# Kernel tuning notes

Measured on AMD Instinct MI355X. Metric: run time of the kernel, lower is better.

The kernel has to match this reference:

```python
import jax, jax.numpy as jnp
import numpy as np

NUM_HEADS = 32
NUM_KV_HEADS = 8
HEAD_DIM = 128
ROPE_THETA = 1000000.0
SCALING = HEAD_DIM ** -0.5


def apply_rope_neox(x, positions):
    # x: [T, H, D], positions: [T] int
    half = HEAD_DIM // 2
    inv_freq = 1.0 / (ROPE_THETA ** (jnp.arange(0, half, dtype=jnp.float32) / half))
    freqs = positions.astype(jnp.float32)[:, None] * inv_freq[None, :]  # [T, D/2]
    cos = jnp.cos(freqs)[:, None, :]  # [T, 1, D/2]
    sin = jnp.sin(freqs)[:, None, :]
    x1, x2 = x[..., :half], x[..., half:]
    return jnp.concatenate([x1 * cos - x2 * sin, x2 * cos + x1 * sin], axis=-1)


def setup_inputs() -> dict:
    key = jax.random.key(0)
    k1, k2, k3 = jax.random.split(key, 3)
    T, H = 2048, 4096
    positions = jnp.arange(T, dtype=jnp.int32)
    hidden_states = jax.random.normal(k1, (T, H), dtype=jnp.float32)
    Wqkv = jax.random.normal(k2, (H, 6144), dtype=jnp.float32) * 0.02
    Wo = jax.random.normal(k3, (H, H), dtype=jnp.float32) * 0.02
    return {"positions": positions, "hidden_states": hidden_states, "Wqkv": Wqkv, "Wo": Wo}


def reference(positions, hidden_states, Wqkv, Wo):
    T = hidden_states.shape[0]
    q_size = NUM_HEADS * HEAD_DIM
    kv_size = NUM_KV_HEADS * HEAD_DIM
    qkv = hidden_states @ Wqkv  # [T, 6144]
    q = qkv[:, :q_size].reshape(T, NUM_HEADS, HEAD_DIM)
    k = qkv[:, q_size:q_size + kv_size].reshape(T, NUM_KV_HEADS, HEAD_DIM)
    v = qkv[:, q_size + kv_size:].reshape(T, NUM_KV_HEADS, HEAD_DIM)
    q = apply_rope_neox(q, positions)
    k = apply_rope_neox(k, positions)
    # GQA: repeat kv heads to match query heads
    rep = NUM_HEADS // NUM_KV_HEADS
    k = jnp.repeat(k, rep, axis=1)  # [T, H, D]
    v = jnp.repeat(v, rep, axis=1)
    scores = jnp.einsum('thd,shd->hts', q, k) * SCALING  # [H, T, T]
    causal = jnp.tril(jnp.ones((T, T), dtype=bool))
    scores = jnp.where(causal[None], scores, jnp.finfo(scores.dtype).min)
    attn = jax.nn.softmax(scores, axis=-1)
    out = jnp.einsum('hts,shd->thd', attn, v).reshape(T, NUM_HEADS * HEAD_DIM)
    return out @ Wo
```

## Files before the change

### kernel.cpp

```cpp
#include <hip/hip_runtime.h>
#include <math.h>

#define T_TOK 2048
#define HDIM  4096
#define QKVN  6144
#define NHEADS 32
#define HD    128
#define KV_OFF 4096
#define V_OFF  5120
#define SCALE 0.08838834764831843f

typedef __attribute__((ext_vector_type(8))) short short8;
typedef __attribute__((ext_vector_type(4))) float f32x4;
typedef __attribute__((ext_vector_type(16))) float f32x16;

__device__ __forceinline__ ushort f2bf(float f) {
    union { float f; unsigned u; } v; v.f = f;
    unsigned r = v.u + 0x7FFFu + ((v.u >> 16) & 1u);
    return (ushort)(r >> 16);
}

template <int N_, int K_>
__global__ __launch_bounds__(512, 2) void gemm_bf16_8ph(const ushort* __restrict__ A,
                                                        const ushort* __restrict__ B,
                                                        float* __restrict__ C) {
    __shared__ __attribute__((aligned(16))) ushort As[2][2][8192];
    __shared__ __attribute__((aligned(16))) ushort Bs[2][2][8192];

    constexpr int NT = K_ / 64;
    constexpr int NBN = N_ / 256;

    const int nwg = (int)gridDim.x;
    const int bid = (int)blockIdx.x;
    const int swz = (nwg & 7) ? bid : ((bid & 7) * (nwg >> 3) + (bid >> 3));
    const int bm = (swz / NBN) * 256;
    const int bn = (swz % NBN) * 256;

    const int tid = (int)threadIdx.x;
    const int w = tid >> 6;
    const int l = tid & 63;
    const int hfa = w >> 2;
    const int hfb = (w & 3) >> 1;
    const int wbr64 = (w & 1) * 4096;

    const int arc = (l & 15) * 64;
    const int ac0 = ((((l >> 4) << 4)) ^ ((l & 7) << 4)) >> 1;
    const int ac1 = (((1 << 6) | ((l >> 4) << 4)) ^ ((l & 7) << 4)) >> 1;

    const int grow = w * 8 + (l >> 3);
    const int gcol = ((l & 7) ^ (l >> 3)) * 8;
    const ushort* Ag = A + (size_t)(bm + grow) * K_ + gcol;
    const ushort* Bg = B + (size_t)(bn + grow) * K_ + gcol;

    auto ldsA = (__attribute__((address_space(3))) char*)&As[0][0][0];
    auto ldsB = (__attribute__((address_space(3))) char*)&Bs[0][0][0];
    const int wsl = w * 1024;

#define STG2(ldsbase, gsrc, bufi, hfi, kt)                                                              \
    do {                                                                                                \
        __builtin_amdgcn_global_load_lds(                                                               \
            (const __attribute__((address_space(1))) void*)((gsrc) + (size_t)((hfi) * 128) * K_ + (kt) * 64),       \
            (__attribute__((address_space(3))) void*)((ldsbase) + (bufi) * 32768 + (hfi) * 16384 + wsl), 16, 0, 0);  \
        __builtin_amdgcn_global_load_lds(                                                               \
            (const __attribute__((address_space(1))) void*)((gsrc) + (size_t)((hfi) * 128 + 64) * K_ + (kt) * 64),  \
            (__attribute__((address_space(3))) void*)((ldsbase) + (bufi) * 32768 + (hfi) * 16384 + 8192 + wsl), 16, 0, 0); \
    } while (0)

    STG2(ldsB, Bg, 0, 0, 0);
    STG2(ldsB, Bg, 0, 1, 0);
    STG2(ldsA, Ag, 0, 0, 0);
    STG2(ldsA, Ag, 0, 1, 0);
    STG2(ldsB, Bg, 1, 0, 1);
    STG2(ldsB, Bg, 1, 1, 1);
    STG2(ldsA, Ag, 1, 0, 1);
    asm volatile("s_waitcnt vmcnt(6)" ::: "memory");
    __builtin_amdgcn_s_barrier();

    f32x4 acc[8][4];
#pragma unroll
    for (int i = 0; i < 8; i++)
#pragma unroll
        for (int j = 0; j < 4; j++) acc[i][j] = (f32x4){0.f, 0.f, 0.f, 0.f};

    short8 a0[4][2], a1[4][2], bq[4][2];

    int buf = 0;
    for (int t = 0; t < NT; ++t) {
        const int nb = buf ^ 1;
        const ushort* Abuf = &As[buf][hfa][0];
        const ushort* Bbuf = &Bs[buf][hfb][0] + wbr64;

#pragma unroll
        for (int fi = 0; fi < 4; fi++) {
            a0[fi][0] = *(const short8*)(Abuf + fi * 1024 + arc + ac0);
            a0[fi][1] = *(const short8*)(Abuf + fi * 1024 + arc + ac1);
        }
#pragma unroll
        for (int fj = 0; fj < 4; fj++) {
            bq[fj][0] = *(const short8*)(Bbuf + fj * 1024 + arc + ac0);
            bq[fj][1] = *(const short8*)(Bbuf + fj * 1024 + arc + ac1);
        }
        if (t + 1 < NT) STG2(ldsA, Ag, nb, 1, t + 1);
        __builtin_amdgcn_s_barrier();
        __builtin_amdgcn_s_setprio(1);
#pragma unroll
        for (int fi = 0; fi < 4; fi++)
#pragma unroll
            for (int fj = 0; fj < 2; fj++)
#pragma unroll
                for (int s = 0; s < 2; s++)
                    acc[fi][fj] = __builtin_amdgcn_mfma_f32_16x16x32_bf16(a0[fi][s], bq[fj][s], acc[fi][fj], 0, 0, 0);
        __builtin_amdgcn_s_setprio(0);
        __builtin_amdgcn_s_barrier();

        if (t + 2 < NT) STG2(ldsB, Bg, buf, 0, t + 2);
        __builtin_amdgcn_s_barrier();
        __builtin_amdgcn_s_setprio(1);
#pragma unroll
        for (int fi = 0; fi < 4; fi++)
#pragma unroll
            for (int fj = 2; fj < 4; fj++)
#pragma unroll
                for (int s = 0; s < 2; s++)
                    acc[fi][fj] = __builtin_amdgcn_mfma_f32_16x16x32_bf16(a0[fi][s], bq[fj][s], acc[fi][fj], 0, 0, 0);
        __builtin_amdgcn_s_setprio(0);
        __builtin_amdgcn_s_barrier();

#pragma unroll
        for (int fi = 0; fi < 4; fi++) {
            a1[fi][0] = *(const short8*)(Abuf + (fi + 4) * 1024 + arc + ac0);
            a1[fi][1] = *(const short8*)(Abuf + (fi + 4) * 1024 + arc + ac1);
        }
        if (t + 2 < NT) STG2(ldsB, Bg, buf, 1, t + 2);
        __builtin_amdgcn_s_barrier();
        __builtin_amdgcn_s_setprio(1);
#pragma unroll
        for (int fi = 0; fi < 4; fi++)
#pragma unroll
            for (int fj = 2; fj < 4; fj++)
#pragma unroll
                for (int s = 0; s < 2; s++)
                    acc[fi + 4][fj] = __builtin_amdgcn_mfma_f32_16x16x32_bf16(a1[fi][s], bq[fj][s], acc[fi + 4][fj], 0, 0, 0);
        __builtin_amdgcn_s_setprio(0);
        __builtin_amdgcn_s_barrier();

        if (t + 2 < NT) {
            STG2(ldsA, Ag, buf, 0, t + 2);
            asm volatile("s_waitcnt vmcnt(6)" ::: "memory");
        } else {
            asm volatile("s_waitcnt vmcnt(0)" ::: "memory");
        }
        __builtin_amdgcn_s_barrier();
        __builtin_amdgcn_s_setprio(1);
#pragma unroll
        for (int fi = 0; fi < 4; fi++)
#pragma unroll
            for (int fj = 0; fj < 2; fj++)
#pragma unroll
                for (int s = 0; s < 2; s++)
                    acc[fi + 4][fj] = __builtin_amdgcn_mfma_f32_16x16x32_bf16(a1[fi][s], bq[fj][s], acc[fi + 4][fj], 0, 0, 0);
        __builtin_amdgcn_s_setprio(0);
        __builtin_amdgcn_s_barrier();

        buf = nb;
    }
#undef STG2

    const int cn = bn + (w & 3) * 64 + (l & 15);
    const int rm = bm + hfa * 128 + ((l >> 4) << 2);
#pragma unroll
    for (int fi = 0; fi < 8; fi++)
#pragma unroll
        for (int fj = 0; fj < 4; fj++)
#pragma unroll
            for (int r = 0; r < 4; r++)
                C[(size_t)(rm + 16 * fi + r) * N_ + cn + 16 * fj] = acc[fi][fj][r];
}

__global__ __launch_bounds__(256) void cast_bf16(const float* __restrict__ in,
                                                 ushort* __restrict__ outp) {
    const int i = (blockIdx.x * 256 + threadIdx.x) * 4;
    float4 v = *(const float4*)(in + i);
    ushort4 o = {f2bf(v.x), f2bf(v.y), f2bf(v.z), f2bf(v.w)};
    *(ushort4*)(outp + i) = o;
}

template <int K_, int N_>
__global__ __launch_bounds__(256) void transpose_cast(const float* __restrict__ W,
                                                      ushort* __restrict__ WT) {
    __shared__ float T[32 * 65];
    const int k0 = blockIdx.y * 32;
    const int n0 = blockIdx.x * 64;
    const int x = threadIdx.x & 63;
    const int y = threadIdx.x >> 6;
#pragma unroll
    for (int p = 0; p < 8; p++) {
        const int kk = p * 4 + y;
        T[kk * 65 + x] = W[(size_t)(k0 + kk) * N_ + n0 + x];
    }
    __syncthreads();
#pragma unroll
    for (int q = 0; q < 4; q++) {
        const int nl = q * 16 + (threadIdx.x >> 4);
        const int k2 = (threadIdx.x & 15) * 2;
        ushort2 o = {f2bf(T[k2 * 65 + nl]), f2bf(T[(k2 + 1) * 65 + nl])};
        *(ushort2*)&WT[(size_t)(n0 + nl) * K_ + k0 + k2] = o;
    }
}

__global__ __launch_bounds__(256) void rope_cast(const int* __restrict__ pos,
                                                 const float* __restrict__ qkv,
                                                 ushort* __restrict__ qkB) {
    const int t = blockIdx.x;
    const int slot = blockIdx.y * 4 + (threadIdx.x >> 6);
    const int d = threadIdx.x & 63;
    const float p = (float)pos[t];
    const float invf = exp2f(-(float)d * (19.931568569324174f / 64.0f));
    const float f = p * invf;
    const float c = cosf(f), s = sinf(f);
    const float sc = (slot < 32) ? SCALE : 1.0f;
    const float* base = qkv + (size_t)t * QKVN + slot * HD;
    ushort* ob = qkB + (size_t)t * QKVN + slot * HD;
    const float x1 = base[d];
    const float x2 = base[d + 64];
    ob[d]      = f2bf((x1 * c - x2 * s) * sc);
    ob[d + 64] = f2bf((x2 * c + x1 * s) * sc);
}

__global__ __launch_bounds__(256) void vt_cast(const float* __restrict__ qkv,
                                               ushort* __restrict__ Vt) {
    __shared__ float tile[32][33];
    const int t0 = blockIdx.x * 32;
    const int c0 = blockIdx.y * 32;
    const int tx = threadIdx.x & 31;
    const int ty = threadIdx.x >> 5;
#pragma unroll
    for (int i = 0; i < 4; i++) {
        const int tt = ty + 8 * i;
        tile[tt][tx] = qkv[(size_t)(t0 + tt) * QKVN + V_OFF + c0 + tx];
    }
    __syncthreads();
#pragma unroll
    for (int i = 0; i < 4; i++) {
        const int dd = ty + 8 * i;
        Vt[(size_t)(c0 + dd) * 2048 + t0 + tx] = f2bf(tile[tx][dd]);
    }
}

__global__ __launch_bounds__(256, 2) void flash_attn_mfma(
        const ushort* __restrict__ qkB,
        const ushort* __restrict__ Vt,
        ushort* __restrict__ attnB) {
    __shared__ ushort Kf[8 * 512];
    __shared__ ushort Vf[8 * 512];

    const int b = blockIdx.x;
    const int half = b >> 8;
    const int rest = b & 255;
    const int h = rest >> 3;
    const int q8 = rest & 7;
    const int qi = half ? (15 - q8) : q8;
    const int kvh = h >> 2;

    const int tid = threadIdx.x;
    const int w = tid >> 6;
    const int l = tid & 63;
    const int l31 = l & 31;
    const int hf = l >> 5;

    const int qg = qi * 128 + w * 32 + l31;

    short8 qf[8];
    {
        const ushort* qrow = qkB + (size_t)qg * QKVN + h * HD + hf * 8;
#pragma unroll
        for (int kt = 0; kt < 8; kt++)
            qf[kt] = *(const short8*)(qrow + kt * 16);
    }

    f32x16 O[4];
#pragma unroll
    for (int dt = 0; dt < 4; dt++)
#pragma unroll
        for (int r = 0; r < 16; r++) O[dt][r] = 0.f;
    float mcur = -INFINITY, lcur = 0.f;

    const ushort* kbase = qkB + (size_t)l31 * QKVN + KV_OFF + kvh * HD + (2 * w) * 16 + hf * 8;
    const ushort* vbase = Vt + ((size_t)(kvh * 128 + w * 32 + l31)) * 2048 + hf * 8;

    auto ldsK = (__attribute__((address_space(3))) char*)Kf;
    auto ldsV = (__attribute__((address_space(3))) char*)Vf;

    const int nst = 4 * qi + 4;
    const int mylast = 4 * qi + w;

    for (int st = 0; st < nst; st++) {
        __syncthreads();
        {
            const ushort* kg = kbase + (size_t)st * 32 * QKVN;
            __builtin_amdgcn_global_load_lds(
                (const __attribute__((address_space(1))) void*)kg,
                (__attribute__((address_space(3))) void*)(ldsK + (2 * w) * 1024), 16, 0, 0);
            __builtin_amdgcn_global_load_lds(
                (const __attribute__((address_space(1))) void*)(kg + 16),
                (__attribute__((address_space(3))) void*)(ldsK + (2 * w + 1) * 1024), 16, 0, 0);
            const ushort* vg = vbase + st * 32;
            __builtin_amdgcn_global_load_lds(
                (const __attribute__((address_space(1))) void*)vg,
                (__attribute__((address_space(3))) void*)(ldsV + (2 * w) * 1024), 16, 0, 0);
            __builtin_amdgcn_global_load_lds(
                (const __attribute__((address_space(1))) void*)(vg + 16),
                (__attribute__((address_space(3))) void*)(ldsV + (2 * w + 1) * 1024), 16, 0, 0);
        }
        __syncthreads();

        if (st <= mylast) {
            f32x16 S;
#pragma unroll
            for (int r = 0; r < 16; r++) S[r] = 0.f;
#pragma unroll
            for (int kt = 0; kt < 8; kt++) {
                short8 afK = *(const short8*)&Kf[kt * 512 + l * 8];
                S = __builtin_amdgcn_mfma_f32_32x32x16_bf16(afK, qf[kt], S, 0, 0, 0);
            }

            float p[16];
#pragma unroll
            for (int r = 0; r < 16; r++) p[r] = S[r];
            if (st == mylast) {
                const int sb = st * 32 + 4 * hf;
#pragma unroll
                for (int r = 0; r < 16; r++) {
                    const int sg = sb + (r & 3) + 8 * (r >> 2);
                    if (sg > qg) p[r] = -INFINITY;
                }
            }
            float rmax = p[0];
#pragma unroll
            for (int r = 1; r < 16; r++) rmax = fmaxf(rmax, p[r]);
            rmax = fmaxf(rmax, __shfl_xor(rmax, 32));
            const float mnew = fmaxf(mcur, rmax);
            const float alpha = __expf(mcur - mnew);
            float rsum = 0.f;
#pragma unroll
            for (int r = 0; r < 16; r++) {
                p[r] = __expf(p[r] - mnew);
                rsum += p[r];
            }
            rsum += __shfl_xor(rsum, 32);
            lcur = lcur * alpha + rsum;
            mcur = mnew;

#pragma unroll
            for (int dt = 0; dt < 4; dt++)
#pragma unroll
                for (int r = 0; r < 16; r++) O[dt][r] *= alpha;

            unsigned pk[8], rk[8];
#pragma unroll
            for (int g = 0; g < 4; g++) {
                pk[2 * g]     = (unsigned)f2bf(p[4 * g])     | ((unsigned)f2bf(p[4 * g + 1]) << 16);
                pk[2 * g + 1] = (unsigned)f2bf(p[4 * g + 2]) | ((unsigned)f2bf(p[4 * g + 3]) << 16);
            }
#pragma unroll
            for (int i = 0; i < 8; i++) rk[i] = (unsigned)__shfl_xor((int)pk[i], 32);

            short8 Pf[2];
#pragma unroll
            for (int kt2 = 0; kt2 < 2; kt2++) {
                const int g = 2 * kt2 + hf;
                union { unsigned u[4]; short8 s; } cvt;
                cvt.u[0] = hf ? rk[2 * g]     : pk[2 * g];
                cvt.u[1] = hf ? rk[2 * g + 1] : pk[2 * g + 1];
                cvt.u[2] = hf ? pk[2 * g]     : rk[2 * g];
                cvt.u[3] = hf ? pk[2 * g + 1] : rk[2 * g + 1];
                Pf[kt2] = cvt.s;
            }

#pragma unroll
            for (int dt = 0; dt < 4; dt++)
#pragma unroll
                for (int kt2 = 0; kt2 < 2; kt2++) {
                    short8 afV = *(const short8*)&Vf[(dt * 2 + kt2) * 512 + l * 8];
                    O[dt] = __builtin_amdgcn_mfma_f32_32x32x16_bf16(afV, Pf[kt2], O[dt], 0, 0, 0);
                }
        }
    }

    const float inv = 1.0f / lcur;
    ushort* orow = attnB + (size_t)qg * HDIM + h * HD + 4 * hf;
#pragma unroll
    for (int dt = 0; dt < 4; dt++)
#pragma unroll
        for (int rg = 0; rg < 4; rg++) {
            ushort4 o;
            o.x = f2bf(O[dt][4 * rg + 0] * inv);
            o.y = f2bf(O[dt][4 * rg + 1] * inv);
            o.z = f2bf(O[dt][4 * rg + 2] * inv);
            o.w = f2bf(O[dt][4 * rg + 3] * inv);
            *(ushort4*)(orow + dt * 32 + 8 * rg) = o;
        }
}

__global__ __launch_bounds__(256) void rope_kernel(const int* __restrict__ pos,
                                                   float* __restrict__ qkv) {
    const int t = blockIdx.x;
    const int head = blockIdx.y * 4 + (threadIdx.x >> 6);
    const int d = threadIdx.x & 63;
    const float p = (float)pos[t];
    const float invf = exp2f(-(float)d * (19.931568569324174f / 64.0f));
    const float f = p * invf;
    const float c = cosf(f), s = sinf(f);
    float* base = qkv + (size_t)t * QKVN + head * HD;
    const float x1 = base[d];
    const float x2 = base[d + 64];
    base[d]      = x1 * c - x2 * s;
    base[d + 64] = x2 * c + x1 * s;
}

#define DOT4(acc, a, b) acc += (a).x*(b).x + (a).y*(b).y + (a).z*(b).z + (a).w*(b).w
#define FMA4(o, p, v) { (o).x += (p)*(v).x; (o).y += (p)*(v).y; (o).z += (p)*(v).z; (o).w += (p)*(v).w; }

__global__ __launch_bounds__(256, 2) void flash_attn_f32(const float* __restrict__ qkv,
                                                         float* __restrict__ out) {
    __shared__ float Qs[64 * 132];
    __shared__ float KVs[32 * 132];
    __shared__ float Ps[64 * 34];
    const int b = blockIdx.x;
    const int half = (b >> 9) & 1;
    const int rest = b & 511;
    const int h = rest >> 4;
    const int qlo = rest & 15;
    const int qi = half ? (31 - qlo) : qlo;
    const int kvh = h >> 2;
    const int tid = threadIdx.x;
    const int tx = tid & 7;
    const int ty = tid >> 3;
    {
        const float* qbase = qkv + (size_t)(qi * 64) * QKVN + h * HD;
#pragma unroll
        for (int r = 0; r < 8; r++) {
            int idx = r * 256 + tid;
            int qrow = idx >> 5;
            int d = (idx & 31) * 4;
            float4 v = *(const float4*)(qbase + (size_t)qrow * QKVN + d);
            v.x *= SCALE; v.y *= SCALE; v.z *= SCALE; v.w *= SCALE;
            *(float4*)(Qs + qrow * 132 + d) = v;
        }
    }
    float m[2], lsm[2];
    float4 O[2][4];
#pragma unroll
    for (int i = 0; i < 2; i++) {
        m[i] = -INFINITY; lsm[i] = 0.f;
#pragma unroll
        for (int jj = 0; jj < 4; jj++) O[i][jj] = make_float4(0.f, 0.f, 0.f, 0.f);
    }
    const float* kbase = qkv + KV_OFF + kvh * HD;
    const float* vbase = qkv + V_OFF + kvh * HD;
    const int qg0 = qi * 64 + ty;
    const int nst = 2 * qi + 2;
    for (int st = 0; st < nst; st++) {
        __syncthreads();
#pragma unroll
        for (int r = 0; r < 4; r++) {
            int idx = r * 256 + tid;
            int srow = idx >> 5;
            int d = (idx & 31) * 4;
            *(float4*)(KVs + srow * 132 + d) =
                *(const float4*)(kbase + (size_t)(st * 32 + srow) * QKVN + d);
        }
        __syncthreads();
        float S[2][4];
#pragma unroll
        for (int i = 0; i < 2; i++)
#pragma unroll
            for (int j = 0; j < 4; j++) S[i][j] = 0.f;
#pragma unroll 4
        for (int kk = 0; kk < HD; kk += 4) {
            float4 q0 = *(const float4*)(Qs + ty * 132 + kk);
            float4 q1 = *(const float4*)(Qs + (ty + 32) * 132 + kk);
            float4 k0 = *(const float4*)(KVs + tx * 132 + kk);
            float4 k1 = *(const float4*)(KVs + (tx + 8) * 132 + kk);
            float4 k2 = *(const float4*)(KVs + (tx + 16) * 132 + kk);
            float4 k3 = *(const float4*)(KVs + (tx + 24) * 132 + kk);
            DOT4(S[0][0], q0, k0); DOT4(S[0][1], q0, k1);
            DOT4(S[0][2], q0, k2); DOT4(S[0][3], q0, k3);
            DOT4(S[1][0], q1, k0); DOT4(S[1][1], q1, k1);
            DOT4(S[1][2], q1, k2); DOT4(S[1][3], q1, k3);
        }
        const int sg0 = st * 32 + tx;
        float alpha[2];
#pragma unroll
        for (int i = 0; i < 2; i++) {
            const int qg = qg0 + 32 * i;
            float rmax = -INFINITY;
#pragma unroll
            for (int j = 0; j < 4; j++) {
                if (sg0 + 8 * j > qg) S[i][j] = -INFINITY;
                rmax = fmaxf(rmax, S[i][j]);
            }
#pragma unroll
            for (int off = 1; off < 8; off <<= 1)
                rmax = fmaxf(rmax, __shfl_xor(rmax, off));
            const float mnew = fmaxf(m[i], rmax);
            alpha[i] = __expf(m[i] - mnew);
            float rsum = 0.f;
#pragma unroll
            for (int j = 0; j < 4; j++) {
                S[i][j] = __expf(S[i][j] - mnew);
                rsum += S[i][j];
            }
#pragma unroll
            for (int off = 1; off < 8; off <<= 1)
                rsum += __shfl_xor(rsum, off);
            lsm[i] = lsm[i] * alpha[i] + rsum;
            m[i] = mnew;
        }
#pragma unroll
        for (int i = 0; i < 2; i++)
#pragma unroll
            for (int j = 0; j < 4; j++)
                Ps[(ty + 32 * i) * 34 + tx + 8 * j] = S[i][j];
        __syncthreads();
#pragma unroll
        for (int r = 0; r < 4; r++) {
            int idx = r * 256 + tid;
            int srow = idx >> 5;
            int d = (idx & 31) * 4;
            *(float4*)(KVs + srow * 132 + d) =
                *(const float4*)(vbase + (size_t)(st * 32 + srow) * QKVN + d);
        }
        __syncthreads();
#pragma unroll
        for (int i = 0; i < 2; i++) {
            const float a = alpha[i];
#pragma unroll
            for (int jj = 0; jj < 4; jj++) {
                O[i][jj].x *= a; O[i][jj].y *= a; O[i][jj].z *= a; O[i][jj].w *= a;
            }
        }
#pragma unroll 4
        for (int s = 0; s < 32; s++) {
            float p0 = Ps[ty * 34 + s];
            float p1 = Ps[(ty + 32) * 34 + s];
            const float* vr = KVs + s * 132 + 4 * tx;
            float4 v0 = *(const float4*)(vr);
            float4 v1 = *(const float4*)(vr + 32);
            float4 v2 = *(const float4*)(vr + 64);
            float4 v3 = *(const float4*)(vr + 96);
            FMA4(O[0][0], p0, v0); FMA4(O[0][1], p0, v1);
            FMA4(O[0][2], p0, v2); FMA4(O[0][3], p0, v3);
            FMA4(O[1][0], p1, v0); FMA4(O[1][1], p1, v1);
            FMA4(O[1][2], p1, v2); FMA4(O[1][3], p1, v3);
        }
    }
#pragma unroll
    for (int i = 0; i < 2; i++) {
        const float inv = 1.0f / lsm[i];
        float* orow = out + (size_t)(qi * 64 + ty + 32 * i) * HDIM + h * HD + 4 * tx;
#pragma unroll
        for (int jj = 0; jj < 4; jj++) {
            float4 wv = O[i][jj];
            wv.x *= inv; wv.y *= inv; wv.z *= inv; wv.w *= inv;
            *(float4*)(orow + 32 * jj) = wv;
        }
    }
}

template <int N_, int K_>
__global__ __launch_bounds__(256) void sgemm(const float* __restrict__ A,
                                             const float* __restrict__ B,
                                             float* __restrict__ C) {
    __shared__ float As[8][128];
    __shared__ float Bs[8][128];
    const int tid = threadIdx.x;
    const int bm = blockIdx.y * 128;
    const int bn = blockIdx.x * 128;
    const int tx = tid & 15;
    const int ty = tid >> 4;
    const int lm = tid >> 1;
    const int lkq = (tid & 1) * 4;
    const int lr = tid >> 5;
    const int lnq = (tid & 31) * 4;
    float acc[8][8];
#pragma unroll
    for (int i = 0; i < 8; i++)
#pragma unroll
        for (int j = 0; j < 8; j++) acc[i][j] = 0.f;
    const float* Aptr = A + (size_t)(bm + lm) * K_ + lkq;
    const float* Bptr = B + (size_t)lr * N_ + bn + lnq;
    for (int k0 = 0; k0 < K_; k0 += 8) {
        float4 av = *(const float4*)Aptr;
        float4 bv = *(const float4*)Bptr;
        __syncthreads();
        As[lkq + 0][lm] = av.x;
        As[lkq + 1][lm] = av.y;
        As[lkq + 2][lm] = av.z;
        As[lkq + 3][lm] = av.w;
        *(float4*)&Bs[lr][lnq] = bv;
        __syncthreads();
        Aptr += 8;
        Bptr += (size_t)8 * N_;
#pragma unroll
        for (int kk = 0; kk < 8; kk++) {
            float4 a0 = *(const float4*)&As[kk][ty * 4];
            float4 a1 = *(const float4*)&As[kk][64 + ty * 4];
            float4 b0 = *(const float4*)&Bs[kk][tx * 4];
            float4 b1 = *(const float4*)&Bs[kk][64 + tx * 4];
            float a[8] = {a0.x, a0.y, a0.z, a0.w, a1.x, a1.y, a1.z, a1.w};
            float bb[8] = {b0.x, b0.y, b0.z, b0.w, b1.x, b1.y, b1.z, b1.w};
#pragma unroll
            for (int i = 0; i < 8; i++)
#pragma unroll
                for (int j = 0; j < 8; j++) acc[i][j] += a[i] * bb[j];
        }
    }
#pragma unroll
    for (int i = 0; i < 8; i++) {
        int row = bm + ((i < 4) ? (ty * 4 + i) : (64 + ty * 4 + i - 4));
        float4 c0 = {acc[i][0], acc[i][1], acc[i][2], acc[i][3]};
        float4 c1 = {acc[i][4], acc[i][5], acc[i][6], acc[i][7]};
        *(float4*)&C[(size_t)row * N_ + bn + tx * 4] = c0;
        *(float4*)&C[(size_t)row * N_ + bn + 64 + tx * 4] = c1;
    }
}

extern "C" void kernel_launch(void* const* d_in, const int* in_sizes, int n_in,
                              void* d_out, int out_size, void* d_ws, size_t ws_size,
                              hipStream_t stream) {
    const int*   positions = (const int*)d_in[0];
    const float* hidden    = (const float*)d_in[1];
    const float* Wqkv      = (const float*)d_in[2];
    const float* Wo        = (const float*)d_in[3];
    float* out = (float*)d_out;

    char* ws = (char*)d_ws;
    float*  qkv   = (float*)ws;
    ushort* attnB = (ushort*)ws;
    ushort* WqkvT = (ushort*)(ws + 50331648);
    ushort* WoT   = (ushort*)(ws + 100663296);
    ushort* hA    = (ushort*)(ws + 134217728);
    ushort* qkB   = (ushort*)(ws + 134217728);
    ushort* Vt    = (ushort*)(ws + 159383552);
    const size_t NEEDED = 163577856;

    if (ws_size >= NEEDED) {
        cast_bf16<<<dim3((T_TOK * HDIM) / 1024), 256, 0, stream>>>(hidden, hA);
        transpose_cast<HDIM, QKVN><<<dim3(QKVN / 64, HDIM / 32), 256, 0, stream>>>(Wqkv, WqkvT);
        transpose_cast<HDIM, HDIM><<<dim3(HDIM / 64, HDIM / 32), 256, 0, stream>>>(Wo, WoT);
        gemm_bf16_8ph<QKVN, HDIM><<<dim3((T_TOK / 256) * (QKVN / 256)), 512, 0, stream>>>(hA, WqkvT, qkv);
        rope_cast<<<dim3(T_TOK, 10), 256, 0, stream>>>(positions, qkv, qkB);
        vt_cast<<<dim3(T_TOK / 32, 32), 256, 0, stream>>>(qkv, Vt);
        flash_attn_mfma<<<dim3(512), 256, 0, stream>>>(qkB, Vt, attnB);
        gemm_bf16_8ph<HDIM, HDIM><<<dim3((T_TOK / 256) * (HDIM / 256)), 512, 0, stream>>>(attnB, WoT, out);
    } else {
        float* attn = qkv + (size_t)T_TOK * QKVN;
        sgemm<QKVN, HDIM><<<dim3(QKVN / 128, T_TOK / 128), 256, 0, stream>>>(hidden, Wqkv, qkv);
        rope_kernel<<<dim3(T_TOK, 10), 256, 0, stream>>>(positions, qkv);
        flash_attn_f32<<<dim3(1024), 256, 0, stream>>>(qkv, attn);
        sgemm<HDIM, HDIM><<<dim3(HDIM / 128, T_TOK / 128), 256, 0, stream>>>(attn, Wo, out);
    }
}
```

Measured before the change: 671.9 us.

## Prefetch GEMM LDS fragments, split-K output GEMM, double-buffer attention K/V tiles

The bf16 GEMM now loads the next tile's A and B fragments from LDS during the current tile's MFMA phases, adding explicit lgkmcnt waits, so LDS read latency overlaps compute. The output projection GEMM is split into two K halves across blockIdx.y, writing to the output and to a scratch partial buffer that a new add kernel sums. This doubles the number of workgroups for the 128-tile grid. The flash attention kernel double-buffers its K/V LDS tiles with async global-to-LDS loads and raises wave priority around the MFMAs. The cost is an extra full-size read/write pass for the split-K sum and more registers and LDS.

```diff
diff --git a/kernel.cpp b/kernel.cpp
--- a/kernel.cpp
+++ b/kernel.cpp
@@ -20,19 +20,23 @@
     return (ushort)(r >> 16);
 }
 
-template <int N_, int K_>
+template <int N_, int LDK, int KC>
 __global__ __launch_bounds__(512, 2) void gemm_bf16_8ph(const ushort* __restrict__ A,
                                                         const ushort* __restrict__ B,
-                                                        float* __restrict__ C) {
+                                                        float* __restrict__ C0,
+                                                        float* __restrict__ C1) {
     __shared__ __attribute__((aligned(16))) ushort As[2][2][8192];
     __shared__ __attribute__((aligned(16))) ushort Bs[2][2][8192];
 
-    constexpr int NT = K_ / 64;
+    constexpr int NT = KC / 64;
     constexpr int NBN = N_ / 256;
 
-    const int nwg = (int)gridDim.x;
+    const int kz = blockIdx.y;
+    float* __restrict__ C = kz ? C1 : C0;
+
+    const int nwgx = (int)gridDim.x;
     const int bid = (int)blockIdx.x;
-    const int swz = (nwg & 7) ? bid : ((bid & 7) * (nwg >> 3) + (bid >> 3));
+    const int swz = (nwgx & 7) ? bid : ((bid & 7) * (nwgx >> 3) + (bid >> 3));
     const int bm = (swz / NBN) * 256;
     const int bn = (swz % NBN) * 256;
 
@@ -49,8 +53,8 @@
 
     const int grow = w * 8 + (l >> 3);
     const int gcol = ((l & 7) ^ (l >> 3)) * 8;
-    const ushort* Ag = A + (size_t)(bm + grow) * K_ + gcol;
-    const ushort* Bg = B + (size_t)(bn + grow) * K_ + gcol;
+    const ushort* Ag = A + (size_t)kz * KC + (size_t)(bm + grow) * LDK + gcol;
+    const ushort* Bg = B + (size_t)kz * KC + (size_t)(bn + grow) * LDK + gcol;
 
     auto ldsA = (__attribute__((address_space(3))) char*)&As[0][0][0];
     auto ldsB = (__attribute__((address_space(3))) char*)&Bs[0][0][0];
@@ -59,10 +63,10 @@
 #define STG2(ldsbase, gsrc, bufi, hfi, kt)                                                              \
     do {                                                                                                \
         __builtin_amdgcn_global_load_lds(                                                               \
-            (const __attribute__((address_space(1))) void*)((gsrc) + (size_t)((hfi) * 128) * K_ + (kt) * 64),       \
+            (const __attribute__((address_space(1))) void*)((gsrc) + (size_t)((hfi) * 128) * LDK + (kt) * 64),       \
             (__attribute__((address_space(3))) void*)((ldsbase) + (bufi) * 32768 + (hfi) * 16384 + wsl), 16, 0, 0);  \
         __builtin_amdgcn_global_load_lds(                                                               \
-            (const __attribute__((address_space(1))) void*)((gsrc) + (size_t)((hfi) * 128 + 64) * K_ + (kt) * 64),  \
+            (const __attribute__((address_space(1))) void*)((gsrc) + (size_t)((hfi) * 128 + 64) * LDK + (kt) * 64),  \
             (__attribute__((address_space(3))) void*)((ldsbase) + (bufi) * 32768 + (hfi) * 16384 + 8192 + wsl), 16, 0, 0); \
     } while (0)
 
@@ -82,25 +86,37 @@
 #pragma unroll
         for (int j = 0; j < 4; j++) acc[i][j] = (f32x4){0.f, 0.f, 0.f, 0.f};
 
-    short8 a0[4][2], a1[4][2], bq[4][2];
+    short8 a0[4][2], aH[4][2], bq01[2][2], bq23[2][2];
+
+    {
+        const ushort* Abuf = &As[0][hfa][0];
+        const ushort* Bbuf = &Bs[0][hfb][0] + wbr64;
+#pragma unroll
+        for (int fi = 0; fi < 4; fi++) {
+            a0[fi][0] = *(const short8*)(Abuf + fi * 1024 + arc + ac0);
+            a0[fi][1] = *(const short8*)(Abuf + fi * 1024 + arc + ac1);
+        }
+#pragma unroll
+        for (int fj = 0; fj < 2; fj++) {
+            bq01[fj][0] = *(const short8*)(Bbuf + fj * 1024 + arc + ac0);
+            bq01[fj][1] = *(const short8*)(Bbuf + fj * 1024 + arc + ac1);
+        }
+    }
 
     int buf = 0;
     for (int t = 0; t < NT; ++t) {
         const int nb = buf ^ 1;
         const ushort* Abuf = &As[buf][hfa][0];
         const ushort* Bbuf = &Bs[buf][hfb][0] + wbr64;
-
-#pragma unroll
-        for (int fi = 0; fi < 4; fi++) {
-            a0[fi][0] = *(const short8*)(Abuf + fi * 1024 + arc + ac0);
-            a0[fi][1] = *(const short8*)(Abuf + fi * 1024 + arc + ac1);
-        }
-#pragma unroll
-        for (int fj = 0; fj < 4; fj++) {
-            bq[fj][0] = *(const short8*)(Bbuf + fj * 1024 + arc + ac0);
-            bq[fj][1] = *(const short8*)(Bbuf + fj * 1024 + arc + ac1);
-        }
+        const ushort* AbufN = &As[nb][hfa][0];
+        const ushort* BbufN = &Bs[nb][hfb][0] + wbr64;
+
         if (t + 1 < NT) STG2(ldsA, Ag, nb, 1, t + 1);
+#pragma unroll
+        for (int fj = 0; fj < 2; fj++) {
+            bq23[fj][0] = *(const short8*)(Bbuf + (fj + 2) * 1024 + arc + ac0);
+            bq23[fj][1] = *(const short8*)(Bbuf + (fj + 2) * 1024 + arc + ac1);
+        }
         __builtin_amdgcn_s_barrier();
         __builtin_amdgcn_s_setprio(1);
 #pragma unroll
@@ -109,39 +125,47 @@
             for (int fj = 0; fj < 2; fj++)
 #pragma unroll
                 for (int s = 0; s < 2; s++)
-                    acc[fi][fj] = __builtin_amdgcn_mfma_f32_16x16x32_bf16(a0[fi][s], bq[fj][s], acc[fi][fj], 0, 0, 0);
+                    acc[fi][fj] = __builtin_amdgcn_mfma_f32_16x16x32_bf16(a0[fi][s], bq01[fj][s], acc[fi][fj], 0, 0, 0);
         __builtin_amdgcn_s_setprio(0);
+        asm volatile("s_waitcnt lgkmcnt(0)" ::: "memory");
         __builtin_amdgcn_s_barrier();
 
         if (t + 2 < NT) STG2(ldsB, Bg, buf, 0, t + 2);
+#pragma unroll
+        for (int fi = 0; fi < 2; fi++) {
+            aH[fi][0] = *(const short8*)(Abuf + (fi + 4) * 1024 + arc + ac0);
+            aH[fi][1] = *(const short8*)(Abuf + (fi + 4) * 1024 + arc + ac1);
+        }
         __builtin_amdgcn_s_barrier();
         __builtin_amdgcn_s_setprio(1);
 #pragma unroll
         for (int fi = 0; fi < 4; fi++)
 #pragma unroll
-            for (int fj = 2; fj < 4; fj++)
+            for (int fj = 0; fj < 2; fj++)
 #pragma unroll
                 for (int s = 0; s < 2; s++)
-                    acc[fi][fj] = __builtin_amdgcn_mfma_f32_16x16x32_bf16(a0[fi][s], bq[fj][s], acc[fi][fj], 0, 0, 0);
+                    acc[fi][fj + 2] = __builtin_amdgcn_mfma_f32_16x16x32_bf16(a0[fi][s], bq23[fj][s], acc[fi][fj + 2], 0, 0, 0);
         __builtin_amdgcn_s_setprio(0);
-        __builtin_amdgcn_s_barrier();
-
-#pragma unroll
-        for (int fi = 0; fi < 4; fi++) {
-            a1[fi][0] = *(const short8*)(Abuf + (fi + 4) * 1024 + arc + ac0);
-            a1[fi][1] = *(const short8*)(Abuf + (fi + 4) * 1024 + arc + ac1);
-        }
+        asm volatile("s_waitcnt lgkmcnt(0)" ::: "memory");
+        __builtin_amdgcn_s_barrier();
+
         if (t + 2 < NT) STG2(ldsB, Bg, buf, 1, t + 2);
+#pragma unroll
+        for (int fi = 2; fi < 4; fi++) {
+            aH[fi][0] = *(const short8*)(Abuf + (fi + 4) * 1024 + arc + ac0);
+            aH[fi][1] = *(const short8*)(Abuf + (fi + 4) * 1024 + arc + ac1);
+        }
         __builtin_amdgcn_s_barrier();
         __builtin_amdgcn_s_setprio(1);
 #pragma unroll
         for (int fi = 0; fi < 4; fi++)
 #pragma unroll
-            for (int fj = 2; fj < 4; fj++)
+            for (int fj = 0; fj < 2; fj++)
 #pragma unroll
                 for (int s = 0; s < 2; s++)
-                    acc[fi + 4][fj] = __builtin_amdgcn_mfma_f32_16x16x32_bf16(a1[fi][s], bq[fj][s], acc[fi + 4][fj], 0, 0, 0);
+                    acc[fi + 4][fj + 2] = __builtin_amdgcn_mfma_f32_16x16x32_bf16(aH[fi][s], bq23[fj][s], acc[fi + 4][fj + 2], 0, 0, 0);
         __builtin_amdgcn_s_setprio(0);
+        asm volatile("s_waitcnt lgkmcnt(0)" ::: "memory");
         __builtin_amdgcn_s_barrier();
 
         if (t + 2 < NT) {
@@ -151,6 +175,13 @@
             asm volatile("s_waitcnt vmcnt(0)" ::: "memory");
         }
         __builtin_amdgcn_s_barrier();
+        if (t + 1 < NT) {
+#pragma unroll
+            for (int fi = 0; fi < 4; fi++) {
+                a0[fi][0] = *(const short8*)(AbufN + fi * 1024 + arc + ac0);
+                a0[fi][1] = *(const short8*)(AbufN + fi * 1024 + arc + ac1);
+            }
+        }
         __builtin_amdgcn_s_setprio(1);
 #pragma unroll
         for (int fi = 0; fi < 4; fi++)
@@ -158,8 +189,16 @@
             for (int fj = 0; fj < 2; fj++)
 #pragma unroll
                 for (int s = 0; s < 2; s++)
-                    acc[fi + 4][fj] = __builtin_amdgcn_mfma_f32_16x16x32_bf16(a1[fi][s], bq[fj][s], acc[fi + 4][fj], 0, 0, 0);
+                    acc[fi + 4][fj] = __builtin_amdgcn_mfma_f32_16x16x32_bf16(aH[fi][s], bq01[fj][s], acc[fi + 4][fj], 0, 0, 0);
         __builtin_amdgcn_s_setprio(0);
+        if (t + 1 < NT) {
+#pragma unroll
+            for (int fj = 0; fj < 2; fj++) {
+                bq01[fj][0] = *(const short8*)(BbufN + fj * 1024 + arc + ac0);
+                bq01[fj][1] = *(const short8*)(BbufN + fj * 1024 + arc + ac1);
+            }
+        }
+        asm volatile("s_waitcnt lgkmcnt(0)" ::: "memory");
         __builtin_amdgcn_s_barrier();
 
         buf = nb;
@@ -175,6 +214,15 @@
 #pragma unroll
             for (int r = 0; r < 4; r++)
                 C[(size_t)(rm + 16 * fi + r) * N_ + cn + 16 * fj] = acc[fi][fj][r];
+}
+
+__global__ __launch_bounds__(256) void add_f32(float* __restrict__ out,
+                                               const float* __restrict__ p) {
+    const int i = (blockIdx.x * 256 + threadIdx.x) * 4;
+    float4 a = *(const float4*)(out + i);
+    float4 b = *(const float4*)(p + i);
+    a.x += b.x; a.y += b.y; a.z += b.z; a.w += b.w;
+    *(float4*)(out + i) = a;
 }
 
 __global__ __launch_bounds__(256) void cast_bf16(const float* __restrict__ in,
@@ -251,8 +299,8 @@
         const ushort* __restrict__ qkB,
         const ushort* __restrict__ Vt,
         ushort* __restrict__ attnB) {
-    __shared__ ushort Kf[8 * 512];
-    __shared__ ushort Vf[8 * 512];
+    __shared__ ushort Kf[2][8 * 512];
+    __shared__ ushort Vf[2][8 * 512];
 
     const int b = blockIdx.x;
     const int half = b >> 8;
@@ -288,41 +336,56 @@
     const ushort* kbase = qkB + (size_t)l31 * QKVN + KV_OFF + kvh * HD + (2 * w) * 16 + hf * 8;
     const ushort* vbase = Vt + ((size_t)(kvh * 128 + w * 32 + l31)) * 2048 + hf * 8;
 
-    auto ldsK = (__attribute__((address_space(3))) char*)Kf;
-    auto ldsV = (__attribute__((address_space(3))) char*)Vf;
+    auto ldsK = (__attribute__((address_space(3))) char*)&Kf[0][0];
+    auto ldsV = (__attribute__((address_space(3))) char*)&Vf[0][0];
 
     const int nst = 4 * qi + 4;
     const int mylast = 4 * qi + w;
 
+#define AST(s, bb)                                                                               \
+    do {                                                                                         \
+        const ushort* kg = kbase + (size_t)(s) * 32 * QKVN;                                      \
+        __builtin_amdgcn_global_load_lds(                                                        \
+            (const __attribute__((address_space(1))) void*)kg,                                   \
+            (__attribute__((address_space(3))) void*)(ldsK + (bb) * 8192 + (2 * w) * 1024), 16, 0, 0);      \
+        __builtin_amdgcn_global_load_lds(                                                        \
+            (const __attribute__((address_space(1))) void*)(kg + 16),                            \
+            (__attribute__((address_space(3))) void*)(ldsK + (bb) * 8192 + (2 * w + 1) * 1024), 16, 0, 0);  \
+        const ushort* vg = vbase + (s) * 32;                                                     \
+        __builtin_amdgcn_global_load_lds(                                                        \
+            (const __attribute__((address_space(1))) void*)vg,                                   \
+            (__attribute__((address_space(3))) void*)(ldsV + (bb) * 8192 + (2 * w) * 1024), 16, 0, 0);      \
+        __builtin_amdgcn_global_load_lds(                                                        \
+            (const __attribute__((address_space(1))) void*)(vg + 16),                            \
+            (__attribute__((address_space(3))) void*)(ldsV + (bb) * 8192 + (2 * w + 1) * 1024), 16, 0, 0);  \
+    } while (0)
+
+    AST(0, 0);
+
     for (int st = 0; st < nst; st++) {
-        __syncthreads();
-        {
-            const ushort* kg = kbase + (size_t)st * 32 * QKVN;
-            __builtin_amdgcn_global_load_lds(
-                (const __attribute__((address_space(1))) void*)kg,
-                (__attribute__((address_space(3))) void*)(ldsK + (2 * w) * 1024), 16, 0, 0);
-            __builtin_amdgcn_global_load_lds(
-                (const __attribute__((address_space(1))) void*)(kg + 16),
-                (__attribute__((address_space(3))) void*)(ldsK + (2 * w + 1) * 1024), 16, 0, 0);
-            const ushort* vg = vbase + st * 32;
-            __builtin_amdgcn_global_load_lds(
-                (const __attribute__((address_space(1))) void*)vg,
-                (__attribute__((address_space(3))) void*)(ldsV + (2 * w) * 1024), 16, 0, 0);
-            __builtin_amdgcn_global_load_lds(
-                (const __attribute__((address_space(1))) void*)(vg + 16),
-                (__attribute__((address_space(3))) void*)(ldsV + (2 * w + 1) * 1024), 16, 0, 0);
-        }
-        __syncthreads();
+        const int buf = st & 1;
+        __builtin_amdgcn_s_barrier();
+        if (st + 1 < nst) {
+            AST(st + 1, buf ^ 1);
+            asm volatile("s_waitcnt vmcnt(4)" ::: "memory");
+        } else {
+            asm volatile("s_waitcnt vmcnt(0)" ::: "memory");
+        }
+        __builtin_amdgcn_s_barrier();
 
         if (st <= mylast) {
+            const ushort* Kb = &Kf[buf][0];
+            const ushort* Vb = &Vf[buf][0];
             f32x16 S;
 #pragma unroll
             for (int r = 0; r < 16; r++) S[r] = 0.f;
+            __builtin_amdgcn_s_setprio(1);
 #pragma unroll
             for (int kt = 0; kt < 8; kt++) {
-                short8 afK = *(const short8*)&Kf[kt * 512 + l * 8];
+                short8 afK = *(const short8*)(Kb + kt * 512 + l * 8);
                 S = __builtin_amdgcn_mfma_f32_32x32x16_bf16(afK, qf[kt], S, 0, 0, 0);
             }
+            __builtin_amdgcn_s_setprio(0);
 
             float p[16];
 #pragma unroll
@@ -377,15 +440,18 @@
                 Pf[kt2] = cvt.s;
             }
 
+            __builtin_amdgcn_s_setprio(1);
 #pragma unroll
             for (int dt = 0; dt < 4; dt++)
 #pragma unroll
                 for (int kt2 = 0; kt2 < 2; kt2++) {
-                    short8 afV = *(const short8*)&Vf[(dt * 2 + kt2) * 512 + l * 8];
+                    short8 afV = *(const short8*)(Vb + (dt * 2 + kt2) * 512 + l * 8);
                     O[dt] = __builtin_amdgcn_mfma_f32_32x32x16_bf16(afV, Pf[kt2], O[dt], 0, 0, 0);
                 }
-        }
-    }
+            __builtin_amdgcn_s_setprio(0);
+        }
+    }
+#undef AST
 
     const float inv = 1.0f / lcur;
     ushort* orow = attnB + (size_t)qg * HDIM + h * HD + 4 * hf;
@@ -638,6 +704,7 @@
     char* ws = (char*)d_ws;
     float*  qkv   = (float*)ws;
     ushort* attnB = (ushort*)ws;
+    float*  Pk    = (float*)(ws + 16777216);
     ushort* WqkvT = (ushort*)(ws + 50331648);
     ushort* WoT   = (ushort*)(ws + 100663296);
     ushort* hA    = (ushort*)(ws + 134217728);
@@ -649,11 +716,14 @@
         cast_bf16<<<dim3((T_TOK * HDIM) / 1024), 256, 0, stream>>>(hidden, hA);
         transpose_cast<HDIM, QKVN><<<dim3(QKVN / 64, HDIM / 32), 256, 0, stream>>>(Wqkv, WqkvT);
         transpose_cast<HDIM, HDIM><<<dim3(HDIM / 64, HDIM / 32), 256, 0, stream>>>(Wo, WoT);
-        gemm_bf16_8ph<QKVN, HDIM><<<dim3((T_TOK / 256) * (QKVN / 256)), 512, 0, stream>>>(hA, WqkvT, qkv);
+        gemm_bf16_8ph<QKVN, HDIM, HDIM>
+            <<<dim3((T_TOK / 256) * (QKVN / 256), 1), 512, 0, stream>>>(hA, WqkvT, qkv, qkv);
         rope_cast<<<dim3(T_TOK, 10), 256, 0, stream>>>(positions, qkv, qkB);
         vt_cast<<<dim3(T_TOK / 32, 32), 256, 0, stream>>>(qkv, Vt);
         flash_attn_mfma<<<dim3(512), 256, 0, stream>>>(qkB, Vt, attnB);
-        gemm_bf16_8ph<HDIM, HDIM><<<dim3((T_TOK / 256) * (HDIM / 256)), 512, 0, stream>>>(attnB, WoT, out);
+        gemm_bf16_8ph<HDIM, HDIM, HDIM / 2>
+            <<<dim3((T_TOK / 256) * (HDIM / 256), 2), 512, 0, stream>>>(attnB, WoT, out, Pk);
+        add_f32<<<dim3((T_TOK * HDIM) / 1024), 256, 0, stream>>>(out, Pk);
     } else {
         float* attn = qkv + (size_t)T_TOK * QKVN;
         sgemm<QKVN, HDIM><<<dim3(QKVN / 128, T_TOK / 128), 256, 0, stream>>>(hidden, Wqkv, qkv);
```

After: 736.5 us. +9.6%, slower.
